# Kernel tuning notes

Hardware: AMD Instinct MI355X
Metric: run time of the kernel (lower is better)

## Reference

```python
import jax, jax.numpy as jnp
import numpy as np

B, T, HID = 2, 1024, 2048
H, DK, DV = 16, 128, 128
KC = 4          # short-conv kernel size
CHUNK = 64
EPS = 1e-5


def _dwconv_silu(x, w):
    # causal depthwise conv1d + SiLU: x [B,T,C], w [C,K]
    K = w.shape[1]
    xp = jnp.pad(x, ((0, 0), (K - 1, 0), (0, 0)))
    y = sum(xp[:, i:i + x.shape[1], :] * w[:, i] for i in range(K))
    return jax.nn.silu(y)


def _l2norm(x):
    return x * jax.lax.rsqrt(jnp.sum(x * x, -1, keepdims=True) + 1e-6)


def setup_inputs() -> dict:
    key = jax.random.key(0)
    ks = jax.random.split(key, 22)
    std = 0.02
    w = lambda k, s: jax.random.normal(k, s, jnp.float32) * std
    return dict(
        hidden_states=jax.random.normal(ks[0], (B, T, HID), jnp.float32),
        Wq=w(ks[1], (HID, H * DK)),
        Wk=w(ks[2], (HID, H * DK)),
        Wv=w(ks[3], (HID, H * DV)),
        conv_wq=w(ks[4], (H * DK, KC)),
        conv_wk=w(ks[5], (H * DK, KC)),
        conv_wv=w(ks[6], (H * DV, KC)),
        Wgb1=w(ks[7], (HID, DV)), Wgb2=w(ks[8], (DV, H * DK)),
        Wgd1=w(ks[9], (HID, DV)), Wgd2=w(ks[10], (DV, H * DK)),
        Wbb=w(ks[11], (HID, H)), Wbd=w(ks[12], (HID, H)),
        Wlam=w(ks[13], (HID, H)),
        A_log=jnp.log(jax.random.uniform(ks[14], (H,), jnp.float32, 1.0, 16.0)),
        dt_bias=jnp.zeros((H * DK,), jnp.float32),
        Wg1=w(ks[15], (HID, DV)), Wg2=w(ks[16], (DV, H * DV)),
        bg2=jnp.zeros((H * DV,), jnp.float32),
        onorm_w=jnp.ones((DV,), jnp.float32),
        Wo=w(ks[17], (H * DV, HID)),
    )


def _fkda_core(q, k, v, gf, gs, bf, bs):
    # dual-state (fast/slow) gated delta rule.
    # q,k: [B,T,H,DK]; v: [B,T,H,DV]; gf/gs: log-decay [B,T,H,DK]; bf/bs: [B,T,H]
    scale = DK ** -0.5
    tm = lambda x: jnp.moveaxis(x, 1, 0)                 # time-major
    qT, kT, vT = tm(q) * scale, tm(k), tm(v)
    g2 = jnp.stack([tm(gf), tm(gs)], 1)                  # [T,2,B,H,DK]
    b2 = jnp.stack([tm(bf), tm(bs)], 1)                  # [T,2,B,H]
    NC = T // CHUNK
    chunkify = lambda x: x.reshape((NC, CHUNK) + x.shape[1:])
    inputs = tuple(map(chunkify, (qT, kT, vT, g2, b2)))

    def step(S, inp):
        qt, kt, vt, gt, bt = inp                         # S: [2,B,H,DK,DV]
        S = S * jnp.exp(gt)[..., None]                   # per-channel decay on key dim
        mem = jnp.einsum('bhk,sbhkv->sbhv', kt, S)       # current memory readout
        u = bt[..., None] * (vt[None] - mem)             # delta-rule residual write
        S = S + jnp.einsum('bhk,sbhv->sbhkv', kt, u)
        o = jnp.einsum('bhk,sbhkv->sbhv', qt, S)
        return S, o

    @jax.checkpoint
    def chunk_step(S, inp):
        return jax.lax.scan(step, S, inp)

    S0 = jnp.zeros((2, q.shape[0], H, DK, DV), q.dtype)
    _, o = jax.lax.scan(chunk_step, S0, inputs)          # [NC,CHUNK,2,B,H,DV]
    o = o.reshape((T,) + o.shape[2:])
    return jnp.moveaxis(o[:, 0], 0, 1), jnp.moveaxis(o[:, 1], 0, 1)


def reference(hidden_states, Wq, Wk, Wv, conv_wq, conv_wk, conv_wv,
              Wgb1, Wgb2, Wgd1, Wgd2, Wbb, Wbd, Wlam, A_log, dt_bias,
              Wg1, Wg2, bg2, onorm_w, Wo):
    x = hidden_states
    b, t, _ = x.shape
    q = _dwconv_silu(x @ Wq, conv_wq).reshape(b, t, H, DK)
    k = _dwconv_silu(x @ Wk, conv_wk).reshape(b, t, H, DK)
    v = _dwconv_silu(x @ Wv, conv_wv).reshape(b, t, H, DV)
    g_base = ((x @ Wgb1) @ Wgb2).reshape(b, t, H, DK)    # low-rank decay gates
    g_delta = ((x @ Wgd1) @ Wgd2).reshape(b, t, H, DK)
    bb, bd = x @ Wbb, x @ Wbd
    lam = jax.nn.sigmoid(x @ Wlam)                       # [b,t,H] fast/slow mix
    beta_fast = jax.nn.sigmoid(bb + bd)
    beta_slow = jax.nn.sigmoid(bb - bd)
    dtb = dt_bias.reshape(H, DK)
    gate_of = lambda g: -jnp.exp(A_log)[None, None, :, None] * jax.nn.softplus(g + dtb)
    gf = gate_of(g_base + g_delta)                       # fused_kda_gate, fast
    gs = gate_of(g_base - g_delta)                       # slow (share_decay_gate=False)
    q, k = _l2norm(q), _l2norm(k)                        # use_qk_l2norm_in_kernel
    o_f, o_s = _fkda_core(q, k, v, gf, gs, beta_fast, beta_slow)
    o = lam[..., None] * o_f + (1.0 - lam[..., None]) * o_s
    gate = ((x @ Wg1) @ Wg2 + bg2).reshape(b, t, H, DV)
    o = o * jax.lax.rsqrt(jnp.mean(o * o, -1, keepdims=True) + EPS) * onorm_w
    o = o * jax.nn.sigmoid(gate)                         # FusedRMSNormGated(sigmoid)
    return o.reshape(b, t, H * DV) @ Wo
```

## Files before the change

kernel.cpp:

```cpp
#include <hip/hip_runtime.h>
#include <hip/hip_bf16.h>
#include <math.h>
#include <stdint.h>

#define B_   2
#define T_   1024
#define HID_ 2048
#define H_   16
#define DK_  128
#define DV_  128
#define TS_  16

typedef __bf16 bf16;
typedef __attribute__((ext_vector_type(8))) __bf16 bf16x8;
typedef __attribute__((ext_vector_type(4))) float f32x4;
typedef __attribute__((ext_vector_type(2))) float f32x2;

typedef __attribute__((address_space(3))) uint32_t* lds_ptr_t;
typedef const __attribute__((address_space(1))) uint32_t* glb_ptr_t;

__device__ __forceinline__ float sigmoidf_(float x) {
    return 1.0f / (1.0f + __expf(-x));
}

__device__ __forceinline__ void ldg_to_lds16(const void* g, void* lds) {
    __builtin_amdgcn_global_load_lds((glb_ptr_t)(uintptr_t)g,
                                     (lds_ptr_t)(uintptr_t)lds, 16, 0, 0);
}

template <int CTRL>
__device__ __forceinline__ float dpp_ror_add(float x) {
    int yi = __builtin_amdgcn_update_dpp(
        0, __builtin_bit_cast(int, x), CTRL, 0xF, 0xF, true);
    return x + __builtin_bit_cast(float, yi);
}
__device__ __forceinline__ float row16_allreduce(float x) {
    x = dpp_ror_add<0x128>(x);
    x = dpp_ror_add<0x124>(x);
    x = dpp_ror_add<0x122>(x);
    x = dpp_ror_add<0x121>(x);
    return x;
}

__global__ __launch_bounds__(256) void cast_bf16_kernel(
    const float* __restrict__ in, bf16* __restrict__ out)
{
    int i = blockIdx.x * 256 + threadIdx.x;
    float4 a = ((const float4*)in)[2 * i];
    float4 b = ((const float4*)in)[2 * i + 1];
    bf16x8 o;
    o[0] = (bf16)a.x; o[1] = (bf16)a.y; o[2] = (bf16)a.z; o[3] = (bf16)a.w;
    o[4] = (bf16)b.x; o[5] = (bf16)b.y; o[6] = (bf16)b.z; o[7] = (bf16)b.w;
    ((bf16x8*)out)[i] = o;
}

__global__ __launch_bounds__(256) void tcast_kernel(
    const float* __restrict__ W, bf16* __restrict__ Wt, int K, int N)
{
    __shared__ float tile[32][33];
    const int k0 = blockIdx.y * 32, n0 = blockIdx.x * 32;
    const int r = threadIdx.x >> 5, c = threadIdx.x & 31;
    #pragma unroll
    for (int i = 0; i < 4; ++i)
        tile[r + 8 * i][c] = W[(size_t)(k0 + r + 8 * i) * N + n0 + c];
    __syncthreads();
    #pragma unroll
    for (int i = 0; i < 4; ++i)
        Wt[(size_t)(n0 + r + 8 * i) * K + k0 + c] = (bf16)tile[c][r + 8 * i];
}

__global__ __launch_bounds__(256) void tcast_off_kernel(
    const float* __restrict__ W, bf16* __restrict__ Wt,
    int N, int noff, int koff, float sign)
{
    __shared__ float tile[32][33];
    const int k0 = blockIdx.y * 32, n0 = blockIdx.x * 32;
    const int r = threadIdx.x >> 5, c = threadIdx.x & 31;
    #pragma unroll
    for (int i = 0; i < 4; ++i)
        tile[r + 8 * i][c] = W[(size_t)(k0 + r + 8 * i) * N + n0 + c];
    __syncthreads();
    #pragma unroll
    for (int i = 0; i < 4; ++i)
        Wt[(size_t)(noff + n0 + r + 8 * i) * 256 + koff + k0 + c] =
            (bf16)(sign * tile[c][r + 8 * i]);
}

__global__ __launch_bounds__(256) void mfma_gemm_kernel(
    const bf16* __restrict__ A, const bf16* __restrict__ Bt,
    const float* __restrict__ bias, void* __restrict__ Cout,
    int M, int N, int Kfull, int lda, int ldc, int bf16out)
{
    __shared__ bf16 As[128 * 32];
    __shared__ bf16 Bs[128 * 32];

    const int tid  = threadIdx.x;
    const int w    = tid >> 6;
    const int lane = tid & 63;
    const int n0   = blockIdx.x * 128;
    const int m0   = blockIdx.y * 128;
    const int wm   = (w >> 1) * 64;
    const int wn   = (w & 1) * 64;

    const int lr = lane >> 2;
    const int lc = (lane & 3) * 8;

    f32x4 acc[4][4];
    #pragma unroll
    for (int i = 0; i < 4; ++i)
        #pragma unroll
        for (int j = 0; j < 4; ++j) acc[i][j] = (f32x4)0.0f;

    const bf16* ApL = As + (wm + (lane & 15)) * 32 + (lane >> 4) * 8;
    const bf16* BpL = Bs + (wn + (lane & 15)) * 32 + (lane >> 4) * 8;

    for (int k0 = 0; k0 < Kfull; k0 += 32) {
        #pragma unroll
        for (int i = 0; i < 2; ++i) {
            const int rr = (w * 2 + i) * 16 + lr;
            ldg_to_lds16(A  + (size_t)(m0 + rr) * lda   + k0 + lc, As + (w * 2 + i) * 512);
            ldg_to_lds16(Bt + (size_t)(n0 + rr) * Kfull + k0 + lc, Bs + (w * 2 + i) * 512);
        }
        __syncthreads();

        bf16x8 af[4], bfr[4];
        #pragma unroll
        for (int i = 0; i < 4; ++i) af[i]  = *(const bf16x8*)(ApL + i * 16 * 32);
        #pragma unroll
        for (int j = 0; j < 4; ++j) bfr[j] = *(const bf16x8*)(BpL + j * 16 * 32);
        #pragma unroll
        for (int i = 0; i < 4; ++i)
            #pragma unroll
            for (int j = 0; j < 4; ++j)
                acc[i][j] = __builtin_amdgcn_mfma_f32_16x16x32_bf16(
                    af[i], bfr[j], acc[i][j], 0, 0, 0);
        __syncthreads();
    }

    #pragma unroll
    for (int i = 0; i < 4; ++i) {
        const int row = m0 + wm + i * 16 + (lane >> 4) * 4;
        #pragma unroll
        for (int j = 0; j < 4; ++j) {
            const int col = n0 + wn + j * 16 + (lane & 15);
            const float bv = bias ? bias[col] : 0.0f;
            #pragma unroll
            for (int r = 0; r < 4; ++r) {
                float v = acc[i][j][r] + bv;
                if (bf16out) ((bf16*)Cout)[(size_t)(row + r) * ldc + col] = (bf16)v;
                else ((float*)Cout)[(size_t)(row + r) * ldc + col] = v;
            }
        }
    }
}

__global__ __launch_bounds__(256) void midcast_kernel(
    const float* __restrict__ src, bf16* __restrict__ midb)
{
    int i = blockIdx.x * 256 + threadIdx.x;
    int m = i / 96, c4 = i - m * 96;
    float4 v = *(const float4*)(src + (size_t)m * 6528 + 6144 + c4 * 4);
    bf16 o[4] = {(bf16)v.x, (bf16)v.y, (bf16)v.z, (bf16)v.w};
    *(uint64_t*)(midb + (size_t)m * 384 + c4 * 4) = *(uint64_t*)o;
}

__global__ __launch_bounds__(256) void skinny3_kernel(
    const float* __restrict__ x, const float* __restrict__ Wbb,
    const float* __restrict__ Wbd, const float* __restrict__ Wlam,
    float* __restrict__ bb, float* __restrict__ bd, float* __restrict__ lam)
{
    __shared__ float xs[16][128];
    __shared__ float wsh[128][48];
    const int m0  = blockIdx.x * 16;
    const int tid = threadIdx.x;
    const int r = tid >> 4, cg = tid & 15;
    float acc0 = 0.f, acc1 = 0.f, acc2 = 0.f;

    for (int k0 = 0; k0 < HID_; k0 += 128) {
        __syncthreads();
        #pragma unroll
        for (int i = 0; i < 2; ++i) {
            int f = tid + 256 * i;
            int rr = f >> 5, cc = (f & 31) * 4;
            *(float4*)&xs[rr][cc] = *(const float4*)(x + (size_t)(m0 + rr) * HID_ + k0 + cc);
        }
        #pragma unroll
        for (int i = 0; i < 2; ++i) {
            int f = tid + 256 * i;
            int kk = f >> 2, cc = (f & 3) * 4;
            *(float4*)&wsh[kk][cc]      = *(const float4*)(Wbb  + (size_t)(k0 + kk) * 16 + cc);
            *(float4*)&wsh[kk][16 + cc] = *(const float4*)(Wbd  + (size_t)(k0 + kk) * 16 + cc);
            *(float4*)&wsh[kk][32 + cc] = *(const float4*)(Wlam + (size_t)(k0 + kk) * 16 + cc);
        }
        __syncthreads();
        #pragma unroll 8
        for (int kk = 0; kk < 128; ++kk) {
            float xv = xs[r][kk];
            acc0 += xv * wsh[kk][cg];
            acc1 += xv * wsh[kk][16 + cg];
            acc2 += xv * wsh[kk][32 + cg];
        }
    }
    size_t o = (size_t)(m0 + r) * 16 + cg;
    bb[o] = acc0; bd[o] = acc1; lam[o] = acc2;
}

__global__ __launch_bounds__(256) void conv_silu_kernel(
    const float* __restrict__ xin, int ldx, int coloff,
    const float* __restrict__ w, float* __restrict__ yout, int mode)
{
    const int bt  = blockIdx.x;
    const int t   = bt & (T_ - 1);
    const int tid = threadIdx.x;
    const float* xr = xin + (size_t)bt * ldx + coloff;

    float val[8];
    #pragma unroll
    for (int jj = 0; jj < 8; ++jj) {
        int c = tid + 256 * jj;
        float4 wc = *(const float4*)(w + (size_t)c * 4);
        const float* xc = xr + c;
        float acc = wc.w * xc[0];
        if (t >= 1) acc += wc.z * xc[-ldx];
        if (t >= 2) acc += wc.y * xc[-2 * ldx];
        if (t >= 3) acc += wc.x * xc[-3 * ldx];
        val[jj] = acc * sigmoidf_(acc);
    }

    if (mode > 0) {
        __shared__ float red[4][8];
        const int wv = tid >> 6;
        #pragma unroll
        for (int jj = 0; jj < 8; ++jj) {
            float v2 = val[jj] * val[jj];
            #pragma unroll
            for (int m = 1; m < 64; m <<= 1) v2 += __shfl_xor(v2, m);
            if ((tid & 63) == 0) red[wv][jj] = v2;
        }
        __syncthreads();
        const int wb = (tid >> 7) * 2;
        #pragma unroll
        for (int jj = 0; jj < 8; ++jj) {
            float ss = red[wb][jj] + red[wb + 1][jj];
            float sc = rsqrtf(ss + 1e-6f);
            if (mode == 2) sc *= 0.08838834764831845f;
            val[jj] *= sc;
        }
    }

    const size_t row = (size_t)bt * HID_;
    #pragma unroll
    for (int jj = 0; jj < 8; ++jj)
        yout[row + tid + 256 * jj] = val[jj];
}

__global__ __launch_bounds__(256) void decay_gate_kernel(
    float* gfgs, const float* __restrict__ A_log,
    const float* __restrict__ dt_bias)
{
    size_t i = (size_t)blockIdx.x * 256 + threadIdx.x;
    int c = (int)(i & (HID_ - 1));
    size_t m = i >> 11;
    int h = c >> 7;
    float* pf = gfgs + m * 4096 + c;
    float* ps = pf + 2048;
    float na = -__expf(A_log[h]);
    float db = dt_bias[c];
    float xf = *pf + db;
    float xs = *ps + db;
    float spf = (xf > 20.0f) ? xf : log1pf(__expf(xf));
    float sps = (xs > 20.0f) ? xs : log1pf(__expf(xs));
    *pf = __expf(na * spf);
    *ps = __expf(na * sps);
}

struct StepRegs {
    float4 e0, e1, k0, k1, q0, q1;
    float bt, bv;
};

__global__ __launch_bounds__(256) void fkda_kernel(
    const float* __restrict__ qp, const float* __restrict__ kp,
    const float* __restrict__ vp, const float* __restrict__ egf,
    const float* __restrict__ egs, int ldeg,
    const float* __restrict__ bbp, const float* __restrict__ bdp,
    float* __restrict__ ofp, float* __restrict__ osp)
{
    const int bx = blockIdx.x;
    const int bh = bx & 31;
    const int sv = bx >> 5;
    const int b  = bh >> 4;
    const int h  = bh & 15;
    const int s  = sv >> 3;
    const int vc = sv & 7;

    const float* eg = s ? egs : egf;
    float*       op = s ? osp : ofp;
    const float  bsign = s ? -1.0f : 1.0f;

    const int tid  = threadIdx.x;
    const int lane = tid & 63;
    const int w    = tid >> 6;
    const int kseg = lane & 15;
    const int colb = w * 4 + (lane >> 4);

    const size_t base  = (size_t)b * T_ * HID_ + (size_t)h * DK_;
    const size_t baseg = (size_t)b * T_ * ldeg + (size_t)h * DK_;
    const size_t ocol  = base + (size_t)vc * 16 + colb;

    __shared__ float EG[2][TS_ * 128];
    __shared__ float KK[2][TS_ * 128];
    __shared__ float QQ[2][TS_ * 128];
    __shared__ float VV[2][TS_ * 16];
    __shared__ float BT[2][TS_];

    f32x2 S0 = {0.f, 0.f}, S1 = {0.f, 0.f}, S2 = {0.f, 0.f}, S3 = {0.f, 0.f};

    const int l5  = lane & 31;
    const int ttl = lane >> 5;
    const int cg  = (l5 < 16) ? (l5 * 8) : ((l5 - 16) * 8 + 4);
    const int sl  = kseg * 4;

    auto stage_glds = [&](int bi, int t0) {
        #pragma unroll
        for (int i = 0; i < 2; ++i) {
            int n  = w * 2 + i;
            int tt = n * 2 + ttl;
            size_t rq = base  + (size_t)(t0 + tt) * HID_ + cg;
            size_t rg = baseg + (size_t)(t0 + tt) * ldeg + cg;
            ldg_to_lds16(eg + rg, &EG[bi][n * 256]);
            ldg_to_lds16(kp + rq, &KK[bi][n * 256]);
            ldg_to_lds16(qp + rq, &QQ[bi][n * 256]);
        }
        if (tid < 64) {
            int tt2 = tid >> 2, vo = (tid & 3) * 4;
            size_t g = base + (size_t)(t0 + tt2) * HID_ + vc * 16 + vo;
            ldg_to_lds16(vp + g, &VV[bi][0]);
        }
    };

    float bbv = 0.0f, bdv = 0.0f;
    if (tid < TS_) {
        size_t gi = ((size_t)b * T_ + tid) * H_ + h;
        bbv = bbp[gi]; bdv = bdp[gi];
    }
    stage_glds(0, 0);
    if (tid < TS_) BT[0][tid] = sigmoidf_(bbv + bsign * bdv);

    float ooPrev = 0.0f;

    for (int t0 = 0; t0 < T_; t0 += TS_) {
        const int cur = (t0 >> 4) & 1;
        const int nxt = cur ^ 1;
        const bool more = (t0 + TS_) < T_;

        __syncthreads();

        if (more) {
            stage_glds(nxt, t0 + TS_);
            if (tid < TS_) {
                size_t gi = ((size_t)b * T_ + t0 + TS_ + tid) * H_ + h;
                bbv = bbp[gi]; bdv = bdp[gi];
            }
        }

        if (t0) op[ocol + (size_t)(t0 - TS_ + kseg) * HID_] = ooPrev;

        const float* Eb = &EG[cur][sl];
        const float* Kb = &KK[cur][sl];
        const float* Qb = &QQ[cur][sl];
        const float* Vc = &VV[cur][colb];
        const float* Bc = &BT[cur][0];

        float oo = 0.0f;

        auto ldstep = [&](StepRegs& R, int tt) {
            const float* Ep = Eb + tt * 128;
            const float* Kp = Kb + tt * 128;
            const float* Qp = Qb + tt * 128;
            R.e0 = *(const float4*)(Ep);
            R.e1 = *(const float4*)(Ep + 64);
            R.k0 = *(const float4*)(Kp);
            R.k1 = *(const float4*)(Kp + 64);
            R.q0 = *(const float4*)(Qp);
            R.q1 = *(const float4*)(Qp + 64);
            R.bt = Bc[tt];
            R.bv = R.bt * Vc[tt * 16];
        };

        auto compute = [&](const StepRegs& R, int tt) {
            f32x2 e0 = {R.e0.x, R.e0.y}, e1 = {R.e0.z, R.e0.w};
            f32x2 e2 = {R.e1.x, R.e1.y}, e3 = {R.e1.z, R.e1.w};
            f32x2 k0 = {R.k0.x, R.k0.y}, k1 = {R.k0.z, R.k0.w};
            f32x2 k2 = {R.k1.x, R.k1.y}, k3 = {R.k1.z, R.k1.w};
            f32x2 q0 = {R.q0.x, R.q0.y}, q1 = {R.q0.z, R.q0.w};
            f32x2 q2 = {R.q1.x, R.q1.y}, q3 = {R.q1.z, R.q1.w};

            S0 *= e0; S1 *= e1; S2 *= e2; S3 *= e3;
            f32x2 pa = k0 * S0 + k1 * S1;
            f32x2 pb = k2 * S2 + k3 * S3;
            f32x2 ps = pa + pb;
            float p = row16_allreduce(ps.x + ps.y);

            float u = fmaf(-R.bt, p, R.bv);
            f32x2 u2 = {u, u};
            S0 += k0 * u2; S1 += k1 * u2; S2 += k2 * u2; S3 += k3 * u2;
            f32x2 oa = q0 * S0 + q1 * S1;
            f32x2 ob = q2 * S2 + q3 * S3;
            f32x2 om = oa + ob;
            float o = row16_allreduce(om.x + om.y);

            oo = (tt == kseg) ? o : oo;
        };

        StepRegs RA, RB;
        ldstep(RA, 0);
        #pragma unroll
        for (int tp = 0; tp < TS_; tp += 2) {
            ldstep(RB, tp + 1);
            compute(RA, tp);
            if (tp + 2 < TS_) ldstep(RA, tp + 2);
            compute(RB, tp + 1);
        }

        ooPrev = oo;

        if (more && tid < TS_) BT[nxt][tid] = sigmoidf_(bbv + bsign * bdv);
    }

    op[ocol + (size_t)(T_ - TS_ + kseg) * HID_] = ooPrev;
}

__global__ __launch_bounds__(256) void mix_norm_gate_kernel(
    const float* of, const float* os, const float* lam_pre,
    const float* gate, const float* onorm_w, bf16* outp)
{
    const int bt  = blockIdx.x;
    const int tid = threadIdx.x;
    const size_t row = (size_t)bt * HID_;

    float val[8];
    #pragma unroll
    for (int jj = 0; jj < 8; ++jj) {
        int c = tid + 256 * jj;
        int h = c >> 7;
        float l = sigmoidf_(lam_pre[(size_t)bt * H_ + h]);
        val[jj] = l * of[row + c] + (1.0f - l) * os[row + c];
    }

    __shared__ float red[4][8];
    const int wv = tid >> 6;
    #pragma unroll
    for (int jj = 0; jj < 8; ++jj) {
        float v2 = val[jj] * val[jj];
        #pragma unroll
        for (int m = 1; m < 64; m <<= 1) v2 += __shfl_xor(v2, m);
        if ((tid & 63) == 0) red[wv][jj] = v2;
    }
    __syncthreads();
    const int wb = (tid >> 7) * 2;
    #pragma unroll
    for (int jj = 0; jj < 8; ++jj) {
        int c = tid + 256 * jj;
        float ss   = red[wb][jj] + red[wb + 1][jj];
        float mean = ss * (1.0f / 128.0f);
        float sc   = rsqrtf(mean + 1e-5f) * onorm_w[c & 127];
        float g    = sigmoidf_(gate[row + c]);
        outp[row + c] = (bf16)(val[jj] * sc * g);
    }
}

extern "C" void kernel_launch(void* const* d_in, const int* in_sizes, int n_in,
                              void* d_out, int out_size, void* d_ws, size_t ws_size,
                              hipStream_t stream) {
    const float* x       = (const float*)d_in[0];
    const float* Wq      = (const float*)d_in[1];
    const float* Wk      = (const float*)d_in[2];
    const float* Wv      = (const float*)d_in[3];
    const float* conv_wq = (const float*)d_in[4];
    const float* conv_wk = (const float*)d_in[5];
    const float* conv_wv = (const float*)d_in[6];
    const float* Wgb1    = (const float*)d_in[7];
    const float* Wgb2    = (const float*)d_in[8];
    const float* Wgd1    = (const float*)d_in[9];
    const float* Wgd2    = (const float*)d_in[10];
    const float* Wbb     = (const float*)d_in[11];
    const float* Wbd     = (const float*)d_in[12];
    const float* Wlam    = (const float*)d_in[13];
    const float* A_log   = (const float*)d_in[14];
    const float* dt_bias = (const float*)d_in[15];
    const float* Wg1     = (const float*)d_in[16];
    const float* Wg2     = (const float*)d_in[17];
    const float* bg2     = (const float*)d_in[18];
    const float* onorm_w = (const float*)d_in[19];
    const float* Wo      = (const float*)d_in[20];
    float* out = (float*)d_out;

    const size_t M = (size_t)B_ * T_;

    float* ws = (float*)d_ws;
    size_t off = 0;
    auto alloc = [&](size_t nfloats) { float* p = ws + off; off += nfloats; return p; };

    float* bufQKV = alloc(M * 6528);
    float* wqkvTf = alloc((size_t)6528 * HID_ / 2);
    float* xbf    = alloc(M * HID_ / 2);
    float* bufQ   = alloc(M * HID_);
    float* bufK   = alloc(M * HID_);
    float* bufV   = alloc(M * HID_);
    float* bufC   = alloc(M * HID_);
    float* bufD   = alloc(M * HID_);
    float* midbf  = alloc(M * 384 / 2);
    float* bb     = alloc(M * H_);
    float* bd     = alloc(M * H_);
    float* lamp   = alloc(M * H_);

    bf16* xb    = (bf16*)xbf;
    bf16* obf   = (bf16*)xbf;
    bf16* wqkvT = (bf16*)wqkvTf;
    bf16* woT   = wqkvT;
    bf16* wcat  = wqkvT + (size_t)HID_ * HID_;
    bf16* wgate = wcat + (size_t)4096 * 256;
    bf16* midb  = (bf16*)midbf;
    float* gfgs = bufQKV;
    float* bufE = bufQKV + M * 4096;

    dim3 blk(256);
    auto gemm = [&](const bf16* A, const bf16* Bt, const float* bias, void* C,
                    int Mm, int Nn, int Kk, int lda, int ldc, int bf16out) {
        dim3 grid(Nn / 128, Mm / 128);
        mfma_gemm_kernel<<<grid, blk, 0, stream>>>(A, Bt, bias, C, Mm, Nn, Kk,
                                                   lda, ldc, bf16out);
    };
    auto tcast = [&](const float* W, bf16* Wt, int Kk, int Nn) {
        tcast_kernel<<<dim3(Nn / 32, Kk / 32), blk, 0, stream>>>(W, Wt, Kk, Nn);
    };

    cast_bf16_kernel<<<dim3((unsigned)(M * HID_ / 8 / 256)), blk, 0, stream>>>(x, xb);

    tcast(Wq,   wqkvT,                          HID_, HID_);
    tcast(Wk,   wqkvT + (size_t)2048 * HID_,    HID_, HID_);
    tcast(Wv,   wqkvT + (size_t)4096 * HID_,    HID_, HID_);
    tcast(Wgb1, wqkvT + (size_t)6144 * HID_,    HID_, 128);
    tcast(Wgd1, wqkvT + (size_t)6272 * HID_,    HID_, 128);
    tcast(Wg1,  wqkvT + (size_t)6400 * HID_,    HID_, 128);
    gemm(xb, wqkvT, nullptr, bufQKV, (int)M, 6528, HID_, HID_, 6528, 0);

    conv_silu_kernel<<<dim3(B_ * T_), blk, 0, stream>>>(bufQKV, 6528, 0,
        conv_wq, bufQ, 2);
    conv_silu_kernel<<<dim3(B_ * T_), blk, 0, stream>>>(bufQKV, 6528, 2048,
        conv_wk, bufK, 1);
    conv_silu_kernel<<<dim3(B_ * T_), blk, 0, stream>>>(bufQKV, 6528, 4096,
        conv_wv, bufV, 0);

    midcast_kernel<<<dim3((unsigned)(M * 96 / 256)), blk, 0, stream>>>(bufQKV, midb);

    skinny3_kernel<<<dim3((unsigned)(M / 16)), blk, 0, stream>>>(
        x, Wbb, Wbd, Wlam, bb, bd, lamp);

    tcast_off_kernel<<<dim3(64, 4), blk, 0, stream>>>(Wgb2, wcat, HID_, 0,    0,   1.0f);
    tcast_off_kernel<<<dim3(64, 4), blk, 0, stream>>>(Wgd2, wcat, HID_, 0,    128, 1.0f);
    tcast_off_kernel<<<dim3(64, 4), blk, 0, stream>>>(Wgb2, wcat, HID_, 2048, 0,   1.0f);
    tcast_off_kernel<<<dim3(64, 4), blk, 0, stream>>>(Wgd2, wcat, HID_, 2048, 128, -1.0f);
    tcast(Wg2, wgate, 128, HID_);
    tcast(Wo,  woT,   HID_, HID_);
    gemm(midb,       wcat,  nullptr, gfgs, (int)M, 4096, 256, 384, 4096, 0);
    gemm(midb + 256, wgate, bg2,     bufE, (int)M, HID_, 128, 384, HID_, 0);

    decay_gate_kernel<<<dim3((unsigned)(M * HID_ / 256)), blk, 0, stream>>>(
        gfgs, A_log, dt_bias);

    fkda_kernel<<<dim3(512), blk, 0, stream>>>(bufQ, bufK, bufV,
        gfgs, gfgs + 2048, 4096, bb, bd, bufC, bufD);

    mix_norm_gate_kernel<<<dim3(B_ * T_), blk, 0, stream>>>(
        bufC, bufD, lamp, bufE, onorm_w, obf);

    gemm(obf, woT, nullptr, out, (int)M, HID_, HID_, HID_, HID_, 0);
}
```

Before: 695.0 us.

## Merge prep, conv, and decay-gate kernels; add XCD-aware GEMM block remap

Folds the x cast, all weight transpose-casts, and the skinny beta/lambda projection into one multi-role prep kernel. The three conv+SiLU launches and the mid-cast become one kernel, and the decay-gate softplus/exp moves into the gate GEMM epilogue. The GEMM also remaps block indices in groups of 8 to spread tiles across chiplets. The aim is to cut launch count, a full read-modify-write pass over the gate buffer, and idle gaps between small kernels. The cost is a separate weight buffer for woT, which adds workspace, and more branch divergence in the large fused kernels.

```diff
diff --git a/kernel.cpp b/kernel.cpp
--- a/kernel.cpp
+++ b/kernel.cpp
@@ -42,54 +42,111 @@
     return x;
 }
 
-__global__ __launch_bounds__(256) void cast_bf16_kernel(
-    const float* __restrict__ in, bf16* __restrict__ out)
-{
-    int i = blockIdx.x * 256 + threadIdx.x;
-    float4 a = ((const float4*)in)[2 * i];
-    float4 b = ((const float4*)in)[2 * i + 1];
-    bf16x8 o;
-    o[0] = (bf16)a.x; o[1] = (bf16)a.y; o[2] = (bf16)a.z; o[3] = (bf16)a.w;
-    o[4] = (bf16)b.x; o[5] = (bf16)b.y; o[6] = (bf16)b.z; o[7] = (bf16)b.w;
-    ((bf16x8*)out)[i] = o;
-}
-
-__global__ __launch_bounds__(256) void tcast_kernel(
-    const float* __restrict__ W, bf16* __restrict__ Wt, int K, int N)
-{
-    __shared__ float tile[32][33];
-    const int k0 = blockIdx.y * 32, n0 = blockIdx.x * 32;
-    const int r = threadIdx.x >> 5, c = threadIdx.x & 31;
+__device__ __forceinline__ void tile_tcast(
+    float (*tile)[33], const float* __restrict__ W, bf16* __restrict__ Wt,
+    int N, int ldout, int noff, int koff, float sign, int bx, int by, int tid)
+{
+    const int k0 = by * 32, n0 = bx * 32;
+    const int r = tid >> 5, c = tid & 31;
     #pragma unroll
     for (int i = 0; i < 4; ++i)
         tile[r + 8 * i][c] = W[(size_t)(k0 + r + 8 * i) * N + n0 + c];
     __syncthreads();
     #pragma unroll
     for (int i = 0; i < 4; ++i)
-        Wt[(size_t)(n0 + r + 8 * i) * K + k0 + c] = (bf16)tile[c][r + 8 * i];
-}
-
-__global__ __launch_bounds__(256) void tcast_off_kernel(
-    const float* __restrict__ W, bf16* __restrict__ Wt,
-    int N, int noff, int koff, float sign)
+        Wt[(size_t)(noff + n0 + r + 8 * i) * ldout + koff + k0 + c] =
+            (bf16)(sign * tile[c][r + 8 * i]);
+}
+
+__global__ __launch_bounds__(256) void prep_kernel(
+    const float* __restrict__ x, bf16* __restrict__ xb,
+    const float* __restrict__ Wq, const float* __restrict__ Wk,
+    const float* __restrict__ Wv, const float* __restrict__ Wgb1,
+    const float* __restrict__ Wgd1, const float* __restrict__ Wg1,
+    const float* __restrict__ Wg2, const float* __restrict__ Wo,
+    const float* __restrict__ Wgb2, const float* __restrict__ Wgd2,
+    bf16* __restrict__ wqkvT, bf16* __restrict__ wgate, bf16* __restrict__ woT,
+    bf16* __restrict__ wcat,
+    const float* __restrict__ Wbb, const float* __restrict__ Wbd,
+    const float* __restrict__ Wlam,
+    float* __restrict__ bb, float* __restrict__ bd, float* __restrict__ lam)
 {
     __shared__ float tile[32][33];
-    const int k0 = blockIdx.y * 32, n0 = blockIdx.x * 32;
-    const int r = threadIdx.x >> 5, c = threadIdx.x & 31;
-    #pragma unroll
-    for (int i = 0; i < 4; ++i)
-        tile[r + 8 * i][c] = W[(size_t)(k0 + r + 8 * i) * N + n0 + c];
-    __syncthreads();
-    #pragma unroll
-    for (int i = 0; i < 4; ++i)
-        Wt[(size_t)(noff + n0 + r + 8 * i) * 256 + koff + k0 + c] =
-            (bf16)(sign * tile[c][r + 8 * i]);
+    __shared__ float xs[16][128];
+    __shared__ float wsh[128][48];
+
+    const int bid = blockIdx.x;
+    const int tid = threadIdx.x;
+
+    if (bid < 2048) {
+        int i = bid * 256 + tid;
+        float4 a = ((const float4*)x)[2 * i];
+        float4 b = ((const float4*)x)[2 * i + 1];
+        bf16x8 o;
+        o[0] = (bf16)a.x; o[1] = (bf16)a.y; o[2] = (bf16)a.z; o[3] = (bf16)a.w;
+        o[4] = (bf16)b.x; o[5] = (bf16)b.y; o[6] = (bf16)b.z; o[7] = (bf16)b.w;
+        ((bf16x8*)xb)[i] = o;
+        return;
+    }
+    if (bid < 20480) {
+        int local;
+        const float* src; bf16* dst; int N, ldout, noff = 0, koff = 0, nx;
+        float sign = 1.0f;
+        if      (bid < 6144)  { local = bid - 2048;  src = Wq;   dst = wqkvT;                       N = 2048; ldout = 2048; nx = 64; }
+        else if (bid < 10240) { local = bid - 6144;  src = Wk;   dst = wqkvT + (size_t)2048 * 2048; N = 2048; ldout = 2048; nx = 64; }
+        else if (bid < 14336) { local = bid - 10240; src = Wv;   dst = wqkvT + (size_t)4096 * 2048; N = 2048; ldout = 2048; nx = 64; }
+        else if (bid < 14592) { local = bid - 14336; src = Wgb1; dst = wqkvT + (size_t)6144 * 2048; N = 128;  ldout = 2048; nx = 4;  }
+        else if (bid < 14848) { local = bid - 14592; src = Wgd1; dst = wqkvT + (size_t)6272 * 2048; N = 128;  ldout = 2048; nx = 4;  }
+        else if (bid < 15104) { local = bid - 14848; src = Wg1;  dst = wqkvT + (size_t)6400 * 2048; N = 128;  ldout = 2048; nx = 4;  }
+        else if (bid < 15360) { local = bid - 15104; src = Wg2;  dst = wgate; N = 2048; ldout = 128; nx = 64; }
+        else if (bid < 19456) { local = bid - 15360; src = Wo;   dst = woT;   N = 2048; ldout = 2048; nx = 64; }
+        else if (bid < 19712) { local = bid - 19456; src = Wgb2; dst = wcat; N = 2048; ldout = 256; noff = 0;    koff = 0;   nx = 64; }
+        else if (bid < 19968) { local = bid - 19712; src = Wgd2; dst = wcat; N = 2048; ldout = 256; noff = 0;    koff = 128; nx = 64; }
+        else if (bid < 20224) { local = bid - 19968; src = Wgb2; dst = wcat; N = 2048; ldout = 256; noff = 2048; koff = 0;   nx = 64; }
+        else                  { local = bid - 20224; src = Wgd2; dst = wcat; N = 2048; ldout = 256; noff = 2048; koff = 128; sign = -1.0f; nx = 64; }
+        tile_tcast(tile, src, dst, N, ldout, noff, koff, sign, local % nx, local / nx, tid);
+        return;
+    }
+    {
+        const int m0 = (bid - 20480) * 16;
+        const int r = tid >> 4, cg = tid & 15;
+        float acc0 = 0.f, acc1 = 0.f, acc2 = 0.f;
+        for (int k0 = 0; k0 < HID_; k0 += 128) {
+            __syncthreads();
+            #pragma unroll
+            for (int i = 0; i < 2; ++i) {
+                int f = tid + 256 * i;
+                int rr = f >> 5, cc = (f & 31) * 4;
+                *(float4*)&xs[rr][cc] = *(const float4*)(x + (size_t)(m0 + rr) * HID_ + k0 + cc);
+            }
+            #pragma unroll
+            for (int i = 0; i < 2; ++i) {
+                int f = tid + 256 * i;
+                int kk = f >> 2, cc = (f & 3) * 4;
+                *(float4*)&wsh[kk][cc]      = *(const float4*)(Wbb  + (size_t)(k0 + kk) * 16 + cc);
+                *(float4*)&wsh[kk][16 + cc] = *(const float4*)(Wbd  + (size_t)(k0 + kk) * 16 + cc);
+                *(float4*)&wsh[kk][32 + cc] = *(const float4*)(Wlam + (size_t)(k0 + kk) * 16 + cc);
+            }
+            __syncthreads();
+            #pragma unroll 8
+            for (int kk = 0; kk < 128; ++kk) {
+                float xv = xs[r][kk];
+                acc0 += xv * wsh[kk][cg];
+                acc1 += xv * wsh[kk][16 + cg];
+                acc2 += xv * wsh[kk][32 + cg];
+            }
+        }
+        size_t o = (size_t)(m0 + r) * 16 + cg;
+        bb[o] = acc0; bd[o] = acc1; lam[o] = acc2;
+    }
 }
 
 __global__ __launch_bounds__(256) void mfma_gemm_kernel(
     const bf16* __restrict__ A, const bf16* __restrict__ Bt,
     const float* __restrict__ bias, void* __restrict__ Cout,
-    int M, int N, int Kfull, int lda, int ldc, int bf16out)
+    int M, int N, int Kfull, int lda, int ldc,
+    const float* __restrict__ alog, const float* __restrict__ dtb,
+    int decay_epi)
 {
     __shared__ bf16 As[128 * 32];
     __shared__ bf16 Bs[128 * 32];
@@ -97,10 +154,16 @@
     const int tid  = threadIdx.x;
     const int w    = tid >> 6;
     const int lane = tid & 63;
-    const int n0   = blockIdx.x * 128;
-    const int m0   = blockIdx.y * 128;
-    const int wm   = (w >> 1) * 64;
-    const int wn   = (w & 1) * 64;
+
+    const int gx  = gridDim.x;
+    const int nwg = gx * gridDim.y;
+    int f = blockIdx.y * gx + blockIdx.x;
+    if ((nwg & 7) == 0) { int q = nwg >> 3; f = (f & 7) * q + (f >> 3); }
+    const int n0 = (f % gx) * 128;
+    const int m0 = (f / gx) * 128;
+
+    const int wm = (w >> 1) * 64;
+    const int wn = (w & 1) * 64;
 
     const int lr = lane >> 2;
     const int lc = (lane & 3) * 8;
@@ -137,81 +200,40 @@
         __syncthreads();
     }
 
+    float* Cf = (float*)Cout;
     #pragma unroll
     for (int i = 0; i < 4; ++i) {
         const int row = m0 + wm + i * 16 + (lane >> 4) * 4;
         #pragma unroll
         for (int j = 0; j < 4; ++j) {
             const int col = n0 + wn + j * 16 + (lane & 15);
-            const float bv = bias ? bias[col] : 0.0f;
-            #pragma unroll
-            for (int r = 0; r < 4; ++r) {
-                float v = acc[i][j][r] + bv;
-                if (bf16out) ((bf16*)Cout)[(size_t)(row + r) * ldc + col] = (bf16)v;
-                else ((float*)Cout)[(size_t)(row + r) * ldc + col] = v;
+            if (decay_epi) {
+                const int c  = col & (HID_ - 1);
+                const int hh = c >> 7;
+                const float na = -__expf(alog[hh]);
+                const float db = dtb[c];
+                #pragma unroll
+                for (int r = 0; r < 4; ++r) {
+                    float xv = acc[i][j][r] + db;
+                    float sp = (xv > 20.0f) ? xv : log1pf(__expf(xv));
+                    Cf[(size_t)(row + r) * ldc + col] = __expf(na * sp);
+                }
+            } else {
+                const float bv = bias ? bias[col] : 0.0f;
+                #pragma unroll
+                for (int r = 0; r < 4; ++r)
+                    Cf[(size_t)(row + r) * ldc + col] = acc[i][j][r] + bv;
             }
         }
     }
 }
 
-__global__ __launch_bounds__(256) void midcast_kernel(
-    const float* __restrict__ src, bf16* __restrict__ midb)
-{
-    int i = blockIdx.x * 256 + threadIdx.x;
-    int m = i / 96, c4 = i - m * 96;
-    float4 v = *(const float4*)(src + (size_t)m * 6528 + 6144 + c4 * 4);
-    bf16 o[4] = {(bf16)v.x, (bf16)v.y, (bf16)v.z, (bf16)v.w};
-    *(uint64_t*)(midb + (size_t)m * 384 + c4 * 4) = *(uint64_t*)o;
-}
-
-__global__ __launch_bounds__(256) void skinny3_kernel(
-    const float* __restrict__ x, const float* __restrict__ Wbb,
-    const float* __restrict__ Wbd, const float* __restrict__ Wlam,
-    float* __restrict__ bb, float* __restrict__ bd, float* __restrict__ lam)
-{
-    __shared__ float xs[16][128];
-    __shared__ float wsh[128][48];
-    const int m0  = blockIdx.x * 16;
-    const int tid = threadIdx.x;
-    const int r = tid >> 4, cg = tid & 15;
-    float acc0 = 0.f, acc1 = 0.f, acc2 = 0.f;
-
-    for (int k0 = 0; k0 < HID_; k0 += 128) {
-        __syncthreads();
-        #pragma unroll
-        for (int i = 0; i < 2; ++i) {
-            int f = tid + 256 * i;
-            int rr = f >> 5, cc = (f & 31) * 4;
-            *(float4*)&xs[rr][cc] = *(const float4*)(x + (size_t)(m0 + rr) * HID_ + k0 + cc);
-        }
-        #pragma unroll
-        for (int i = 0; i < 2; ++i) {
-            int f = tid + 256 * i;
-            int kk = f >> 2, cc = (f & 3) * 4;
-            *(float4*)&wsh[kk][cc]      = *(const float4*)(Wbb  + (size_t)(k0 + kk) * 16 + cc);
-            *(float4*)&wsh[kk][16 + cc] = *(const float4*)(Wbd  + (size_t)(k0 + kk) * 16 + cc);
-            *(float4*)&wsh[kk][32 + cc] = *(const float4*)(Wlam + (size_t)(k0 + kk) * 16 + cc);
-        }
-        __syncthreads();
-        #pragma unroll 8
-        for (int kk = 0; kk < 128; ++kk) {
-            float xv = xs[r][kk];
-            acc0 += xv * wsh[kk][cg];
-            acc1 += xv * wsh[kk][16 + cg];
-            acc2 += xv * wsh[kk][32 + cg];
-        }
-    }
-    size_t o = (size_t)(m0 + r) * 16 + cg;
-    bb[o] = acc0; bd[o] = acc1; lam[o] = acc2;
-}
-
-__global__ __launch_bounds__(256) void conv_silu_kernel(
-    const float* __restrict__ xin, int ldx, int coloff,
-    const float* __restrict__ w, float* __restrict__ yout, int mode)
-{
-    const int bt  = blockIdx.x;
-    const int t   = bt & (T_ - 1);
-    const int tid = threadIdx.x;
+__device__ __forceinline__ void conv_body(
+    float (*red)[8], const float* __restrict__ xin, int ldx, int coloff,
+    const float* __restrict__ w, float* __restrict__ yout, int mode,
+    int bt, int tid)
+{
+    const int t = bt & (T_ - 1);
     const float* xr = xin + (size_t)bt * ldx + coloff;
 
     float val[8];
@@ -228,7 +250,6 @@
     }
 
     if (mode > 0) {
-        __shared__ float red[4][8];
         const int wv = tid >> 6;
         #pragma unroll
         for (int jj = 0; jj < 8; ++jj) {
@@ -254,24 +275,26 @@
         yout[row + tid + 256 * jj] = val[jj];
 }
 
-__global__ __launch_bounds__(256) void decay_gate_kernel(
-    float* gfgs, const float* __restrict__ A_log,
-    const float* __restrict__ dt_bias)
-{
-    size_t i = (size_t)blockIdx.x * 256 + threadIdx.x;
-    int c = (int)(i & (HID_ - 1));
-    size_t m = i >> 11;
-    int h = c >> 7;
-    float* pf = gfgs + m * 4096 + c;
-    float* ps = pf + 2048;
-    float na = -__expf(A_log[h]);
-    float db = dt_bias[c];
-    float xf = *pf + db;
-    float xs = *ps + db;
-    float spf = (xf > 20.0f) ? xf : log1pf(__expf(xf));
-    float sps = (xs > 20.0f) ? xs : log1pf(__expf(xs));
-    *pf = __expf(na * spf);
-    *ps = __expf(na * sps);
+__global__ __launch_bounds__(256) void convmid_kernel(
+    const float* __restrict__ xin,
+    const float* __restrict__ wq, const float* __restrict__ wk,
+    const float* __restrict__ wv,
+    float* __restrict__ bufQ, float* __restrict__ bufK,
+    float* __restrict__ bufV, bf16* __restrict__ midb)
+{
+    __shared__ float red[4][8];
+    const int bid = blockIdx.x;
+    const int tid = threadIdx.x;
+    if (bid < 2048)      conv_body(red, xin, 6528, 0,    wq, bufQ, 2, bid,        tid);
+    else if (bid < 4096) conv_body(red, xin, 6528, 2048, wk, bufK, 1, bid - 2048, tid);
+    else if (bid < 6144) conv_body(red, xin, 6528, 4096, wv, bufV, 0, bid - 4096, tid);
+    else {
+        int i = (bid - 6144) * 256 + tid;
+        int m = i / 96, c4 = i - m * 96;
+        float4 v = *(const float4*)(xin + (size_t)m * 6528 + 6144 + c4 * 4);
+        bf16 o[4] = {(bf16)v.x, (bf16)v.y, (bf16)v.z, (bf16)v.w};
+        *(uint64_t*)(midb + (size_t)m * 384 + c4 * 4) = *(uint64_t*)o;
+    }
 }
 
 struct StepRegs {
@@ -502,8 +525,9 @@
     size_t off = 0;
     auto alloc = [&](size_t nfloats) { float* p = ws + off; off += nfloats; return p; };
 
-    float* bufQKV = alloc(M * 6528);
-    float* wqkvTf = alloc((size_t)6528 * HID_ / 2);
+    float* bufQKV  = alloc(M * 6528);
+    float* wqkvTf  = alloc((size_t)6528 * HID_ / 2);
+    float* wextraf = alloc(((size_t)4096 * 256 + 2048 * 128 + (size_t)2048 * 2048) / 2);
     float* xbf    = alloc(M * HID_ / 2);
     float* bufQ   = alloc(M * HID_);
     float* bufK   = alloc(M * HID_);
@@ -518,57 +542,37 @@
     bf16* xb    = (bf16*)xbf;
     bf16* obf   = (bf16*)xbf;
     bf16* wqkvT = (bf16*)wqkvTf;
-    bf16* woT   = wqkvT;
-    bf16* wcat  = wqkvT + (size_t)HID_ * HID_;
+    bf16* wcat  = (bf16*)wextraf;
     bf16* wgate = wcat + (size_t)4096 * 256;
+    bf16* woT   = wgate + (size_t)2048 * 128;
     bf16* midb  = (bf16*)midbf;
     float* gfgs = bufQKV;
     float* bufE = bufQKV + M * 4096;
 
     dim3 blk(256);
     auto gemm = [&](const bf16* A, const bf16* Bt, const float* bias, void* C,
-                    int Mm, int Nn, int Kk, int lda, int ldc, int bf16out) {
+                    int Mm, int Nn, int Kk, int lda, int ldc,
+                    const float* alog, const float* dtb, int depi) {
         dim3 grid(Nn / 128, Mm / 128);
         mfma_gemm_kernel<<<grid, blk, 0, stream>>>(A, Bt, bias, C, Mm, Nn, Kk,
-                                                   lda, ldc, bf16out);
+                                                   lda, ldc, alog, dtb, depi);
     };
-    auto tcast = [&](const float* W, bf16* Wt, int Kk, int Nn) {
-        tcast_kernel<<<dim3(Nn / 32, Kk / 32), blk, 0, stream>>>(W, Wt, Kk, Nn);
-    };
-
-    cast_bf16_kernel<<<dim3((unsigned)(M * HID_ / 8 / 256)), blk, 0, stream>>>(x, xb);
-
-    tcast(Wq,   wqkvT,                          HID_, HID_);
-    tcast(Wk,   wqkvT + (size_t)2048 * HID_,    HID_, HID_);
-    tcast(Wv,   wqkvT + (size_t)4096 * HID_,    HID_, HID_);
-    tcast(Wgb1, wqkvT + (size_t)6144 * HID_,    HID_, 128);
-    tcast(Wgd1, wqkvT + (size_t)6272 * HID_,    HID_, 128);
-    tcast(Wg1,  wqkvT + (size_t)6400 * HID_,    HID_, 128);
-    gemm(xb, wqkvT, nullptr, bufQKV, (int)M, 6528, HID_, HID_, 6528, 0);
-
-    conv_silu_kernel<<<dim3(B_ * T_), blk, 0, stream>>>(bufQKV, 6528, 0,
-        conv_wq, bufQ, 2);
-    conv_silu_kernel<<<dim3(B_ * T_), blk, 0, stream>>>(bufQKV, 6528, 2048,
-        conv_wk, bufK, 1);
-    conv_silu_kernel<<<dim3(B_ * T_), blk, 0, stream>>>(bufQKV, 6528, 4096,
-        conv_wv, bufV, 0);
-
-    midcast_kernel<<<dim3((unsigned)(M * 96 / 256)), blk, 0, stream>>>(bufQKV, midb);
-
-    skinny3_kernel<<<dim3((unsigned)(M / 16)), blk, 0, stream>>>(
-        x, Wbb, Wbd, Wlam, bb, bd, lamp);
-
-    tcast_off_kernel<<<dim3(64, 4), blk, 0, stream>>>(Wgb2, wcat, HID_, 0,    0,   1.0f);
-    tcast_off_kernel<<<dim3(64, 4), blk, 0, stream>>>(Wgd2, wcat, HID_, 0,    128, 1.0f);
-    tcast_off_kernel<<<dim3(64, 4), blk, 0, stream>>>(Wgb2, wcat, HID_, 2048, 0,   1.0f);
-    tcast_off_kernel<<<dim3(64, 4), blk, 0, stream>>>(Wgd2, wcat, HID_, 2048, 128, -1.0f);
-    tcast(Wg2, wgate, 128, HID_);
-    tcast(Wo,  woT,   HID_, HID_);
-    gemm(midb,       wcat,  nullptr, gfgs, (int)M, 4096, 256, 384, 4096, 0);
-    gemm(midb + 256, wgate, bg2,     bufE, (int)M, HID_, 128, 384, HID_, 0);
-
-    decay_gate_kernel<<<dim3((unsigned)(M * HID_ / 256)), blk, 0, stream>>>(
-        gfgs, A_log, dt_bias);
+
+    prep_kernel<<<dim3(20608), blk, 0, stream>>>(
+        x, xb, Wq, Wk, Wv, Wgb1, Wgd1, Wg1, Wg2, Wo, Wgb2, Wgd2,
+        wqkvT, wgate, woT, wcat, Wbb, Wbd, Wlam, bb, bd, lamp);
+
+    gemm(xb, wqkvT, nullptr, bufQKV, (int)M, 6528, HID_, HID_, 6528,
+         nullptr, nullptr, 0);
+
+    convmid_kernel<<<dim3(6912), blk, 0, stream>>>(
+        bufQKV, conv_wq, conv_wk, conv_wv, bufQ, bufK, bufV, midb);
+
+    gemm(midb, wcat, nullptr, gfgs, (int)M, 4096, 256, 384, 4096,
+         A_log, dt_bias, 1);
+
+    gemm(midb + 256, wgate, bg2, bufE, (int)M, HID_, 128, 384, HID_,
+         nullptr, nullptr, 0);
 
     fkda_kernel<<<dim3(512), blk, 0, stream>>>(bufQ, bufK, bufV,
         gfgs, gfgs + 2048, 4096, bb, bd, bufC, bufD);
@@ -576,5 +580,6 @@
     mix_norm_gate_kernel<<<dim3(B_ * T_), blk, 0, stream>>>(
         bufC, bufD, lamp, bufE, onorm_w, obf);
 
-    gemm(obf, woT, nullptr, out, (int)M, HID_, HID_, HID_, HID_, 0);
-}
+    gemm(obf, woT, nullptr, out, (int)M, HID_, HID_, HID_, HID_,
+         nullptr, nullptr, 0);
+}
```

Measured after the change: 718.4 us. 1.03x slower.
